# Kernel optimization log

Hardware: AMD Instinct MI355X
Metric: run time of the kernel (lower is better)

Reference implementation:

```python
import jax, jax.numpy as jnp
import numpy as np

B, N, DIM = 8, 1024, 768
HEADS, DHEAD = 12, 64
INNER = HEADS * DHEAD  # 768
ALPHA = 0.25
SCALE = DHEAD ** -0.5
EPS = 1e-5


def setup_inputs() -> dict:
    key = jax.random.key(0)
    ks = jax.random.split(key, 7)
    x = jax.random.normal(ks[0], (B, N, DIM), dtype=jnp.float32)
    h = jax.random.normal(ks[1], (B, HEADS, N, N), dtype=jnp.float32)
    gamma = jnp.ones((DIM,), dtype=jnp.float32)
    beta = jnp.zeros((DIM,), dtype=jnp.float32)
    w_qkv = jax.random.normal(ks[2], (DIM, 3 * INNER), dtype=jnp.float32) * (DIM ** -0.5)
    w_out = jax.random.normal(ks[3], (INNER, DIM), dtype=jnp.float32) * (INNER ** -0.5)
    b_out = jnp.zeros((DIM,), dtype=jnp.float32)
    return {"x": x, "h": h, "gamma": gamma, "beta": beta,
            "w_qkv": w_qkv, "w_out": w_out, "b_out": b_out}


def reference(x, h, gamma, beta, w_qkv, w_out, b_out):
    # LayerNorm over last dim
    mu = jnp.mean(x, axis=-1, keepdims=True)
    var = jnp.mean(jnp.square(x - mu), axis=-1, keepdims=True)
    xn = (x - mu) * jax.lax.rsqrt(var + EPS) * gamma + beta
    # fused QKV projection (no bias)
    qkv = xn @ w_qkv                                     # (b, n, 3*inner)
    q, k, v = jnp.split(qkv, 3, axis=-1)
    split_heads = lambda t: t.reshape(B, N, HEADS, DHEAD).transpose(0, 2, 1, 3)  # b h n d
    q, k, v = split_heads(q), split_heads(k), split_heads(v)
    raw = jnp.einsum('bhid,bhjd->bhij', q, k) * SCALE    # (b, h, n, n)
    blended = ALPHA * raw + (1.0 - ALPHA) * h
    attn = jax.nn.softmax(blended, axis=-1)              # dropout p=0 -> identity
    out = jnp.einsum('bhij,bhjd->bhid', attn, v)         # (b, h, n, d)
    out = out.transpose(0, 2, 1, 3).reshape(B, N, INNER)
    out = out @ w_out + b_out
    return (out, blended)
```

## Files before the change

kernel.cpp:

```cpp
#include <hip/hip_runtime.h>
#include <hip/hip_bf16.h>
#include <stdint.h>

#define NB 8
#define NSEQ 1024
#define DIMM 768
#define NHEADS 12
#define DH 64
#define NQKV 2304
#define ALPHA_ 0.25f
#define SCALE_ 0.125f
#define EPS_ 1e-5f

typedef __bf16 bf16;
typedef bf16 bf16x8 __attribute__((ext_vector_type(8)));
typedef bf16 bf16x4 __attribute__((ext_vector_type(4)));
typedef float f32x4 __attribute__((ext_vector_type(4)));

#define MFMA16(a, b, c) __builtin_amdgcn_mfma_f32_16x16x32_bf16((a), (b), (c), 0, 0, 0)

static __device__ __forceinline__ void load_lds16(const void* gsrc, void* ldst) {
  __builtin_amdgcn_global_load_lds(
      (__attribute__((address_space(1))) void*)gsrc,
      (__attribute__((address_space(3))) void*)ldst, 16, 0, 0);
}

#define BAR_LGKM()                                             \
  do {                                                         \
    __builtin_amdgcn_sched_barrier(0);                         \
    asm volatile("s_waitcnt lgkmcnt(0)" ::: "memory");         \
    __builtin_amdgcn_s_barrier();                              \
    __builtin_amdgcn_sched_barrier(0);                         \
  } while (0)

static __device__ __forceinline__ int swz(int row, int cb) {
  return cb ^ ((((row & 7) ^ ((cb >> 7) & 7)) << 4));
}

__global__ __launch_bounds__(256) void ln_kernel(
    const float* __restrict__ x, const float* __restrict__ gamma,
    const float* __restrict__ beta, bf16* __restrict__ xn) {
  const int row = blockIdx.x * 4 + (threadIdx.x >> 6);
  const int lane = threadIdx.x & 63;
  const float* xr = x + (size_t)row * DIMM;
  float4 v[3];
  float s = 0.f, s2 = 0.f;
#pragma unroll
  for (int c = 0; c < 3; ++c) {
    v[c] = *reinterpret_cast<const float4*>(xr + c * 256 + lane * 4);
    s += v[c].x + v[c].y + v[c].z + v[c].w;
    s2 += v[c].x * v[c].x + v[c].y * v[c].y + v[c].z * v[c].z + v[c].w * v[c].w;
  }
#pragma unroll
  for (int m = 1; m < 64; m <<= 1) {
    s += __shfl_xor(s, m);
    s2 += __shfl_xor(s2, m);
  }
  const float mu = s * (1.f / DIMM);
  const float rstd = rsqrtf(s2 * (1.f / DIMM) - mu * mu + EPS_);
#pragma unroll
  for (int c = 0; c < 3; ++c) {
    const float4 g4 = *reinterpret_cast<const float4*>(gamma + c * 256 + lane * 4);
    const float4 b4 = *reinterpret_cast<const float4*>(beta + c * 256 + lane * 4);
    bf16x4 o;
    o[0] = (bf16)((v[c].x - mu) * rstd * g4.x + b4.x);
    o[1] = (bf16)((v[c].y - mu) * rstd * g4.y + b4.y);
    o[2] = (bf16)((v[c].z - mu) * rstd * g4.z + b4.z);
    o[3] = (bf16)((v[c].w - mu) * rstd * g4.w + b4.w);
    *reinterpret_cast<bf16x4*>(xn + (size_t)row * DIMM + c * 256 + lane * 4) = o;
  }
}

__global__ __launch_bounds__(256) void tcast_kernel(
    const float* __restrict__ in, bf16* __restrict__ out, int R, int C) {
  __shared__ float tile[32][33];
  const int tx = threadIdx.x & 31, ty = threadIdx.x >> 5;
  const int c0 = blockIdx.x * 32, r0 = blockIdx.y * 32;
#pragma unroll
  for (int i = ty; i < 32; i += 8)
    tile[i][tx] = in[(size_t)(r0 + i) * C + c0 + tx];
  __syncthreads();
#pragma unroll
  for (int i = ty; i < 32; i += 8)
    out[(size_t)(c0 + i) * R + r0 + tx] = (bf16)tile[tx][i];
}

__global__ __launch_bounds__(256) void qkv_gemm(
    const bf16* __restrict__ xn, const bf16* __restrict__ wT,
    bf16* __restrict__ qb, bf16* __restrict__ kb, bf16* __restrict__ vt) {
  __shared__ __align__(16) bf16 As[128 * 32];
  __shared__ __align__(16) bf16 Bs[128 * 32];
  const int tid = threadIdx.x;
  const int wv = tid >> 6, l = tid & 63;
  const int l16 = l & 15, q4 = l >> 4;
  const int wr = wv >> 1, wc = wv & 1;
  const int c0 = blockIdx.x * 128, row0 = blockIdx.y * 128;
  const int sr = tid >> 2, skk = (tid & 3) * 8;
  f32x4 acc[4][4];
#pragma unroll
  for (int m = 0; m < 4; ++m)
#pragma unroll
    for (int n = 0; n < 4; ++n) acc[m][n] = f32x4{0.f, 0.f, 0.f, 0.f};
  for (int k0 = 0; k0 < DIMM; k0 += 32) {
    __syncthreads();
    load_lds16(xn + (size_t)(row0 + sr) * DIMM + k0 + skk, As + tid * 8);
    load_lds16(xn + (size_t)(row0 + 64 + sr) * DIMM + k0 + skk, As + 2048 + tid * 8);
    load_lds16(wT + (size_t)(c0 + sr) * DIMM + k0 + skk, Bs + tid * 8);
    load_lds16(wT + (size_t)(c0 + 64 + sr) * DIMM + k0 + skk, Bs + 2048 + tid * 8);
    __syncthreads();
    bf16x8 a[4], b[4];
#pragma unroll
    for (int m = 0; m < 4; ++m)
      a[m] = *reinterpret_cast<const bf16x8*>(&As[(wr * 64 + m * 16 + l16) * 32 + q4 * 8]);
#pragma unroll
    for (int n = 0; n < 4; ++n)
      b[n] = *reinterpret_cast<const bf16x8*>(&Bs[(wc * 64 + n * 16 + l16) * 32 + q4 * 8]);
#pragma unroll
    for (int m = 0; m < 4; ++m)
#pragma unroll
      for (int n = 0; n < 4; ++n) acc[m][n] = MFMA16(a[m], b[n], acc[m][n]);
  }
  const int sect = c0 / DIMM;
#pragma unroll
  for (int n = 0; n < 4; ++n) {
    const int gc = c0 + wc * 64 + n * 16 + l16;
    const int head = (gc % DIMM) >> 6;
    const int dd = gc & 63;
#pragma unroll
    for (int m = 0; m < 4; ++m) {
#pragma unroll
      for (int r = 0; r < 4; ++r) {
        const int gm = row0 + wr * 64 + m * 16 + q4 * 4 + r;
        const int b_ = gm >> 10, nn = gm & 1023;
        const size_t bhh = (size_t)b_ * NHEADS + head;
        const bf16 val = (bf16)acc[m][n][r];
        if (sect == 0)      qb[(bhh * NSEQ + nn) * DH + dd] = val;
        else if (sect == 1) kb[(bhh * NSEQ + nn) * DH + dd] = val;
        else                vt[(bhh * DH + dd) * NSEQ + nn] = val;
      }
    }
  }
}

__global__ __launch_bounds__(256, 4) void attn_kernel(
    const bf16* __restrict__ qb, const bf16* __restrict__ kb,
    const bf16* __restrict__ vt, const float* __restrict__ h,
    float* __restrict__ blended, bf16* __restrict__ attn_out) {
  __shared__ __align__(16) char S_lds[16 * 2176];
  __shared__ float lred[16];

  const int tid = threadIdx.x;
  const int wv = tid >> 6, l = tid & 63;
  const int l16 = l & 15, q4 = l >> 4;
  const int i0 = blockIdx.x * 16;
  const int bh = blockIdx.y;
  const int jb = wv * 256;

  const float* hbase = h + ((size_t)bh << 20);
  float* bbase = blended + ((size_t)bh << 20);

  bf16x8 qT[2];
#pragma unroll
  for (int w2 = 0; w2 < 2; ++w2)
    qT[w2] = *reinterpret_cast<const bf16x8*>(
        qb + ((size_t)bh * NSEQ + i0 + l16) * DH + w2 * 32 + q4 * 8);

  float4 hv0[4], hv1[4];
#pragma unroll
  for (int t = 0; t < 4; ++t) {
    hv0[t] = *reinterpret_cast<const float4*>(
        hbase + (size_t)(i0 + wv * 4 + 0) * NSEQ + t * 256 + l * 4);
    hv1[t] = *reinterpret_cast<const float4*>(
        hbase + (size_t)(i0 + wv * 4 + 1) * NSEQ + t * 256 + l * 4);
  }

  const bf16* kq = kb + ((size_t)bh * NSEQ + jb + l16) * DH + q4 * 8;
  char* srow_w = S_lds + l16 * 2176;
#pragma unroll
  for (int st = 0; st < 4; ++st) {
    f32x4 s[4];
#pragma unroll
    for (int js = 0; js < 4; ++js) s[js] = f32x4{0.f, 0.f, 0.f, 0.f};
#pragma unroll
    for (int js = 0; js < 4; ++js) {
#pragma unroll
      for (int w2 = 0; w2 < 2; ++w2) {
        const bf16x8 kf = *reinterpret_cast<const bf16x8*>(
            kq + (size_t)(st * 64 + js * 16) * DH + w2 * 32);
        s[js] = MFMA16(kf, qT[w2], s[js]);
      }
    }
#pragma unroll
    for (int js = 0; js < 4; ++js) {
      bf16x4 pk;
#pragma unroll
      for (int r = 0; r < 4; ++r) pk[r] = (bf16)(s[js][r] * (ALPHA_ * SCALE_));
      const int cb = (jb + st * 64 + js * 16 + q4 * 4) * 2;
      *reinterpret_cast<bf16x4*>(srow_w + swz(l16, cb)) = pk;
    }
  }

  float4 hv2[4], hv3[4];
#pragma unroll
  for (int t = 0; t < 4; ++t) {
    hv2[t] = *reinterpret_cast<const float4*>(
        hbase + (size_t)(i0 + wv * 4 + 2) * NSEQ + t * 256 + l * 4);
    hv3[t] = *reinterpret_cast<const float4*>(
        hbase + (size_t)(i0 + wv * 4 + 3) * NSEQ + t * 256 + l * 4);
  }

  BAR_LGKM();

  auto ROW = [&](int rr, float4* hv) {
    const int row = wv * 4 + rr;
    char* srow = S_lds + row * 2176;
    bf16x4 sv[4];
#pragma unroll
    for (int t = 0; t < 4; ++t)
      sv[t] = *reinterpret_cast<const bf16x4*>(srow + swz(row, t * 512 + l * 8));
    float4 bl[4];
    float tm = -1e30f;
#pragma unroll
    for (int t = 0; t < 4; ++t) {
      bl[t].x = fmaf(0.75f, hv[t].x, (float)sv[t][0]);
      bl[t].y = fmaf(0.75f, hv[t].y, (float)sv[t][1]);
      bl[t].z = fmaf(0.75f, hv[t].z, (float)sv[t][2]);
      bl[t].w = fmaf(0.75f, hv[t].w, (float)sv[t][3]);
      *reinterpret_cast<float4*>(
          bbase + (size_t)(i0 + row) * NSEQ + t * 256 + l * 4) = bl[t];
      tm = fmaxf(tm, fmaxf(fmaxf(bl[t].x, bl[t].y), fmaxf(bl[t].z, bl[t].w)));
    }
#pragma unroll
    for (int mm = 1; mm < 64; mm <<= 1) tm = fmaxf(tm, __shfl_xor(tm, mm));
    float rs = 0.f;
#pragma unroll
    for (int t = 0; t < 4; ++t) {
      bf16x4 pk;
      const float p0 = __expf(bl[t].x - tm); rs += p0; pk[0] = (bf16)p0;
      const float p1 = __expf(bl[t].y - tm); rs += p1; pk[1] = (bf16)p1;
      const float p2 = __expf(bl[t].z - tm); rs += p2; pk[2] = (bf16)p2;
      const float p3 = __expf(bl[t].w - tm); rs += p3; pk[3] = (bf16)p3;
      *reinterpret_cast<bf16x4*>(srow + swz(row, t * 512 + l * 8)) = pk;
    }
#pragma unroll
    for (int mm = 1; mm < 64; mm <<= 1) rs += __shfl_xor(rs, mm);
    if (l == 0) lred[row] = rs;
  };
  ROW(0, hv0);
  ROW(1, hv1);
  ROW(2, hv2);
  ROW(3, hv3);

  BAR_LGKM();

  const bf16* vq = vt + ((size_t)bh * DH + wv * 16 + l16) * NSEQ + q4 * 8;
  char* prow = S_lds + l16 * 2176;
  f32x4 a0 = f32x4{0.f, 0.f, 0.f, 0.f}, a1 = a0, a2 = a0, a3 = a0;
#pragma unroll
  for (int ks = 0; ks < 32; ks += 4) {
    const bf16x8 pa0 = *reinterpret_cast<const bf16x8*>(prow + swz(l16, (ks + 0) * 64 + q4 * 16));
    const bf16x8 vf0 = *reinterpret_cast<const bf16x8*>(vq + (ks + 0) * 32);
    a0 = MFMA16(pa0, vf0, a0);
    const bf16x8 pa1 = *reinterpret_cast<const bf16x8*>(prow + swz(l16, (ks + 1) * 64 + q4 * 16));
    const bf16x8 vf1 = *reinterpret_cast<const bf16x8*>(vq + (ks + 1) * 32);
    a1 = MFMA16(pa1, vf1, a1);
    const bf16x8 pa2 = *reinterpret_cast<const bf16x8*>(prow + swz(l16, (ks + 2) * 64 + q4 * 16));
    const bf16x8 vf2 = *reinterpret_cast<const bf16x8*>(vq + (ks + 2) * 32);
    a2 = MFMA16(pa2, vf2, a2);
    const bf16x8 pa3 = *reinterpret_cast<const bf16x8*>(prow + swz(l16, (ks + 3) * 64 + q4 * 16));
    const bf16x8 vf3 = *reinterpret_cast<const bf16x8*>(vq + (ks + 3) * 32);
    a3 = MFMA16(pa3, vf3, a3);
  }
  const f32x4 af = (a0 + a1) + (a2 + a3);
  const int b = bh / NHEADS, head = bh % NHEADS;
#pragma unroll
  for (int r = 0; r < 4; ++r) {
    const int q = q4 * 4 + r;
    attn_out[((size_t)b * NSEQ + i0 + q) * DIMM + head * DH + wv * 16 + l16] =
        (bf16)(af[r] / lred[q]);
  }
}

__global__ __launch_bounds__(256) void oproj_gemm(
    const bf16* __restrict__ ain, const bf16* __restrict__ wT,
    const float* __restrict__ bias, float* __restrict__ out) {
  __shared__ __align__(16) bf16 As[128 * 32];
  __shared__ __align__(16) bf16 Bs[128 * 32];
  const int tid = threadIdx.x;
  const int wv = tid >> 6, l = tid & 63;
  const int l16 = l & 15, q4 = l >> 4;
  const int wr = wv >> 1, wc = wv & 1;
  const int c0 = blockIdx.x * 128, row0 = blockIdx.y * 128;
  const int sr = tid >> 2, skk = (tid & 3) * 8;
  f32x4 acc[4][4];
#pragma unroll
  for (int m = 0; m < 4; ++m)
#pragma unroll
    for (int n = 0; n < 4; ++n) acc[m][n] = f32x4{0.f, 0.f, 0.f, 0.f};
  for (int k0 = 0; k0 < DIMM; k0 += 32) {
    __syncthreads();
    load_lds16(ain + (size_t)(row0 + sr) * DIMM + k0 + skk, As + tid * 8);
    load_lds16(ain + (size_t)(row0 + 64 + sr) * DIMM + k0 + skk, As + 2048 + tid * 8);
    load_lds16(wT + (size_t)(c0 + sr) * DIMM + k0 + skk, Bs + tid * 8);
    load_lds16(wT + (size_t)(c0 + 64 + sr) * DIMM + k0 + skk, Bs + 2048 + tid * 8);
    __syncthreads();
    bf16x8 a[4], b[4];
#pragma unroll
    for (int m = 0; m < 4; ++m)
      a[m] = *reinterpret_cast<const bf16x8*>(&As[(wr * 64 + m * 16 + l16) * 32 + q4 * 8]);
#pragma unroll
    for (int n = 0; n < 4; ++n)
      b[n] = *reinterpret_cast<const bf16x8*>(&Bs[(wc * 64 + n * 16 + l16) * 32 + q4 * 8]);
#pragma unroll
    for (int m = 0; m < 4; ++m)
#pragma unroll
      for (int n = 0; n < 4; ++n) acc[m][n] = MFMA16(a[m], b[n], acc[m][n]);
  }
#pragma unroll
  for (int n = 0; n < 4; ++n) {
    const int gc = c0 + wc * 64 + n * 16 + l16;
    const float bv = bias[gc];
#pragma unroll
    for (int m = 0; m < 4; ++m) {
#pragma unroll
      for (int r = 0; r < 4; ++r) {
        const int gm = row0 + wr * 64 + m * 16 + q4 * 4 + r;
        out[(size_t)gm * DIMM + gc] = acc[m][n][r] + bv;
      }
    }
  }
}

extern "C" void kernel_launch(void* const* d_in, const int* in_sizes, int n_in,
                              void* d_out, int out_size, void* d_ws, size_t ws_size,
                              hipStream_t stream) {
  const float* x = (const float*)d_in[0];
  const float* h = (const float*)d_in[1];
  const float* gamma = (const float*)d_in[2];
  const float* beta = (const float*)d_in[3];
  const float* w_qkv = (const float*)d_in[4];
  const float* w_out = (const float*)d_in[5];
  const float* b_out = (const float*)d_in[6];
  float* out = (float*)d_out;
  float* blended = out + (size_t)NB * NSEQ * DIMM;

  char* ws = (char*)d_ws;
  bf16* xn = (bf16*)(ws);
  bf16* qb = (bf16*)(ws + 12582912);
  bf16* kb = (bf16*)(ws + 25165824);
  bf16* vt = (bf16*)(ws + 37748736);
  bf16* wqkvT = (bf16*)(ws + 50331648);
  bf16* woutT = (bf16*)(ws + 53870592);

  hipLaunchKernelGGL(ln_kernel, dim3(2048), dim3(256), 0, stream, x, gamma, beta, xn);
  hipLaunchKernelGGL(tcast_kernel, dim3(72, 24), dim3(256), 0, stream, w_qkv, wqkvT, DIMM, NQKV);
  hipLaunchKernelGGL(tcast_kernel, dim3(24, 24), dim3(256), 0, stream, w_out, woutT, DIMM, DIMM);
  hipLaunchKernelGGL(qkv_gemm, dim3(18, 64), dim3(256), 0, stream, xn, wqkvT, qb, kb, vt);
  hipLaunchKernelGGL(attn_kernel, dim3(64, 96), dim3(256), 0, stream, qb, kb, vt, h, blended, xn);
  hipLaunchKernelGGL(oproj_gemm, dim3(6, 64), dim3(256), 0, stream, xn, woutT, b_out, out);
}
```

Measured before the change: 388.0 us.

## Split fused attention into score GEMM, blend/softmax-sum, and PV GEMM kernels

```diff
diff --git a/kernel.cpp b/kernel.cpp
--- a/kernel.cpp
+++ b/kernel.cpp
@@ -23,18 +23,6 @@
   __builtin_amdgcn_global_load_lds(
       (__attribute__((address_space(1))) void*)gsrc,
       (__attribute__((address_space(3))) void*)ldst, 16, 0, 0);
-}
-
-#define BAR_LGKM()                                             \
-  do {                                                         \
-    __builtin_amdgcn_sched_barrier(0);                         \
-    asm volatile("s_waitcnt lgkmcnt(0)" ::: "memory");         \
-    __builtin_amdgcn_s_barrier();                              \
-    __builtin_amdgcn_sched_barrier(0);                         \
-  } while (0)
-
-static __device__ __forceinline__ int swz(int row, int cb) {
-  return cb ^ ((((row & 7) ^ ((cb >> 7) & 7)) << 4));
 }
 
 __global__ __launch_bounds__(256) void ln_kernel(
@@ -142,13 +130,9 @@
   }
 }
 
-__global__ __launch_bounds__(256, 4) void attn_kernel(
+__global__ __launch_bounds__(256) void s_gemm(
     const bf16* __restrict__ qb, const bf16* __restrict__ kb,
-    const bf16* __restrict__ vt, const float* __restrict__ h,
-    float* __restrict__ blended, bf16* __restrict__ attn_out) {
-  __shared__ __align__(16) char S_lds[16 * 2176];
-  __shared__ float lred[16];
-
+    float* __restrict__ blended) {
   const int tid = threadIdx.x;
   const int wv = tid >> 6, l = tid & 63;
   const int l16 = l & 15, q4 = l >> 4;
@@ -156,26 +140,14 @@
   const int bh = blockIdx.y;
   const int jb = wv * 256;
 
-  const float* hbase = h + ((size_t)bh << 20);
-  float* bbase = blended + ((size_t)bh << 20);
-
   bf16x8 qT[2];
 #pragma unroll
   for (int w2 = 0; w2 < 2; ++w2)
     qT[w2] = *reinterpret_cast<const bf16x8*>(
         qb + ((size_t)bh * NSEQ + i0 + l16) * DH + w2 * 32 + q4 * 8);
 
-  float4 hv0[4], hv1[4];
-#pragma unroll
-  for (int t = 0; t < 4; ++t) {
-    hv0[t] = *reinterpret_cast<const float4*>(
-        hbase + (size_t)(i0 + wv * 4 + 0) * NSEQ + t * 256 + l * 4);
-    hv1[t] = *reinterpret_cast<const float4*>(
-        hbase + (size_t)(i0 + wv * 4 + 1) * NSEQ + t * 256 + l * 4);
-  }
-
   const bf16* kq = kb + ((size_t)bh * NSEQ + jb + l16) * DH + q4 * 8;
-  char* srow_w = S_lds + l16 * 2176;
+  char* sdst = (char*)blended + (size_t)((bh << 10) + i0 + l16) * 4096;
 #pragma unroll
   for (int st = 0; st < 4; ++st) {
     f32x4 s[4];
@@ -195,89 +167,107 @@
       bf16x4 pk;
 #pragma unroll
       for (int r = 0; r < 4; ++r) pk[r] = (bf16)(s[js][r] * (ALPHA_ * SCALE_));
-      const int cb = (jb + st * 64 + js * 16 + q4 * 4) * 2;
-      *reinterpret_cast<bf16x4*>(srow_w + swz(l16, cb)) = pk;
-    }
-  }
-
-  float4 hv2[4], hv3[4];
-#pragma unroll
-  for (int t = 0; t < 4; ++t) {
-    hv2[t] = *reinterpret_cast<const float4*>(
-        hbase + (size_t)(i0 + wv * 4 + 2) * NSEQ + t * 256 + l * 4);
-    hv3[t] = *reinterpret_cast<const float4*>(
-        hbase + (size_t)(i0 + wv * 4 + 3) * NSEQ + t * 256 + l * 4);
-  }
-
-  BAR_LGKM();
-
-  auto ROW = [&](int rr, float4* hv) {
-    const int row = wv * 4 + rr;
-    char* srow = S_lds + row * 2176;
-    bf16x4 sv[4];
-#pragma unroll
-    for (int t = 0; t < 4; ++t)
-      sv[t] = *reinterpret_cast<const bf16x4*>(srow + swz(row, t * 512 + l * 8));
-    float4 bl[4];
-    float tm = -1e30f;
+      *reinterpret_cast<bf16x4*>(sdst + (jb + st * 64 + js * 16 + q4 * 4) * 2) = pk;
+    }
+  }
+}
+
+__global__ __launch_bounds__(256) void blend_kernel(
+    const float* __restrict__ h, float* __restrict__ blended,
+    float* __restrict__ lsum) {
+  const int l = threadIdx.x & 63;
+  const int w = blockIdx.x * 4 + (threadIdx.x >> 6);
+  float4 hA[4], hB[4];
+  bf16x4 sA[4], sB[4];
+
+  auto LOAD = [&](int rid, float4* hv, bf16x4* sv) {
+    const float* hp = h + (size_t)rid * 1024;
+    const char* sp = (const char*)blended + (size_t)rid * 4096;
+#pragma unroll
+    for (int c = 0; c < 4; ++c) {
+      hv[c] = *reinterpret_cast<const float4*>(hp + c * 256 + l * 4);
+      sv[c] = *reinterpret_cast<const bf16x4*>(sp + (c * 256 + l * 4) * 2);
+    }
+  };
+  auto COMP = [&](int rid, const float4* hv, const bf16x4* sv) {
+    float* bp = blended + (size_t)rid * 1024;
+    float ls = 0.f;
+#pragma unroll
+    for (int c = 0; c < 4; ++c) {
+      float4 b;
+      b.x = fmaf(0.75f, hv[c].x, (float)sv[c][0]);
+      b.y = fmaf(0.75f, hv[c].y, (float)sv[c][1]);
+      b.z = fmaf(0.75f, hv[c].z, (float)sv[c][2]);
+      b.w = fmaf(0.75f, hv[c].w, (float)sv[c][3]);
+      *reinterpret_cast<float4*>(bp + c * 256 + l * 4) = b;
+      ls += __expf(b.x) + __expf(b.y) + __expf(b.z) + __expf(b.w);
+    }
+#pragma unroll
+    for (int mm = 1; mm < 64; mm <<= 1) ls += __shfl_xor(ls, mm);
+    if (l == 0) lsum[rid] = ls;
+  };
+
+  LOAD(w, hA, sA);
+#pragma unroll 1
+  for (int it = 0; it < 16; it += 2) {
+    LOAD(w + (it + 1) * 6144, hB, sB);
+    COMP(w + it * 6144, hA, sA);
+    if (it + 2 < 16) LOAD(w + (it + 2) * 6144, hA, sA);
+    COMP(w + (it + 1) * 6144, hB, sB);
+  }
+}
+
+__global__ __launch_bounds__(256) void pv_gemm(
+    const float* __restrict__ blended, const bf16* __restrict__ vt,
+    const float* __restrict__ lsum, bf16* __restrict__ attn_out) {
+  __shared__ __align__(16) float ored[4 * 16 * 64];
+  const int tid = threadIdx.x;
+  const int wv = tid >> 6, l = tid & 63;
+  const int l16 = l & 15, q4 = l >> 4;
+  const int i0 = blockIdx.x * 16;
+  const int bh = blockIdx.y;
+
+  const float* bq = blended + (size_t)((bh << 10) + i0 + l16) * 1024 + q4 * 8;
+  const bf16* vbase = vt + (size_t)bh * DH * NSEQ + (size_t)q4 * 8;
+
+  f32x4 acc[4];
+#pragma unroll
+  for (int f = 0; f < 4; ++f) acc[f] = f32x4{0.f, 0.f, 0.f, 0.f};
+
+#pragma unroll
+  for (int k8 = 0; k8 < 8; ++k8) {
+    const int ks = wv * 8 + k8;
+    const f32x4 u0 = *reinterpret_cast<const f32x4*>(bq + ks * 32);
+    const f32x4 u1 = *reinterpret_cast<const f32x4*>(bq + ks * 32 + 4);
+    bf16x8 pa;
 #pragma unroll
     for (int t = 0; t < 4; ++t) {
-      bl[t].x = fmaf(0.75f, hv[t].x, (float)sv[t][0]);
-      bl[t].y = fmaf(0.75f, hv[t].y, (float)sv[t][1]);
-      bl[t].z = fmaf(0.75f, hv[t].z, (float)sv[t][2]);
-      bl[t].w = fmaf(0.75f, hv[t].w, (float)sv[t][3]);
-      *reinterpret_cast<float4*>(
-          bbase + (size_t)(i0 + row) * NSEQ + t * 256 + l * 4) = bl[t];
-      tm = fmaxf(tm, fmaxf(fmaxf(bl[t].x, bl[t].y), fmaxf(bl[t].z, bl[t].w)));
-    }
-#pragma unroll
-    for (int mm = 1; mm < 64; mm <<= 1) tm = fmaxf(tm, __shfl_xor(tm, mm));
-    float rs = 0.f;
-#pragma unroll
-    for (int t = 0; t < 4; ++t) {
-      bf16x4 pk;
-      const float p0 = __expf(bl[t].x - tm); rs += p0; pk[0] = (bf16)p0;
-      const float p1 = __expf(bl[t].y - tm); rs += p1; pk[1] = (bf16)p1;
-      const float p2 = __expf(bl[t].z - tm); rs += p2; pk[2] = (bf16)p2;
-      const float p3 = __expf(bl[t].w - tm); rs += p3; pk[3] = (bf16)p3;
-      *reinterpret_cast<bf16x4*>(srow + swz(row, t * 512 + l * 8)) = pk;
-    }
-#pragma unroll
-    for (int mm = 1; mm < 64; mm <<= 1) rs += __shfl_xor(rs, mm);
-    if (l == 0) lred[row] = rs;
-  };
-  ROW(0, hv0);
-  ROW(1, hv1);
-  ROW(2, hv2);
-  ROW(3, hv3);
-
-  BAR_LGKM();
-
-  const bf16* vq = vt + ((size_t)bh * DH + wv * 16 + l16) * NSEQ + q4 * 8;
-  char* prow = S_lds + l16 * 2176;
-  f32x4 a0 = f32x4{0.f, 0.f, 0.f, 0.f}, a1 = a0, a2 = a0, a3 = a0;
-#pragma unroll
-  for (int ks = 0; ks < 32; ks += 4) {
-    const bf16x8 pa0 = *reinterpret_cast<const bf16x8*>(prow + swz(l16, (ks + 0) * 64 + q4 * 16));
-    const bf16x8 vf0 = *reinterpret_cast<const bf16x8*>(vq + (ks + 0) * 32);
-    a0 = MFMA16(pa0, vf0, a0);
-    const bf16x8 pa1 = *reinterpret_cast<const bf16x8*>(prow + swz(l16, (ks + 1) * 64 + q4 * 16));
-    const bf16x8 vf1 = *reinterpret_cast<const bf16x8*>(vq + (ks + 1) * 32);
-    a1 = MFMA16(pa1, vf1, a1);
-    const bf16x8 pa2 = *reinterpret_cast<const bf16x8*>(prow + swz(l16, (ks + 2) * 64 + q4 * 16));
-    const bf16x8 vf2 = *reinterpret_cast<const bf16x8*>(vq + (ks + 2) * 32);
-    a2 = MFMA16(pa2, vf2, a2);
-    const bf16x8 pa3 = *reinterpret_cast<const bf16x8*>(prow + swz(l16, (ks + 3) * 64 + q4 * 16));
-    const bf16x8 vf3 = *reinterpret_cast<const bf16x8*>(vq + (ks + 3) * 32);
-    a3 = MFMA16(pa3, vf3, a3);
-  }
-  const f32x4 af = (a0 + a1) + (a2 + a3);
+      pa[t] = (bf16)__expf(u0[t]);
+      pa[4 + t] = (bf16)__expf(u1[t]);
+    }
+#pragma unroll
+    for (int f = 0; f < 4; ++f) {
+      const bf16x8 vf = *reinterpret_cast<const bf16x8*>(
+          vbase + (size_t)(f * 16 + l16) * NSEQ + ks * 32);
+      acc[f] = MFMA16(pa, vf, acc[f]);
+    }
+  }
+
+#pragma unroll
+  for (int f = 0; f < 4; ++f)
+#pragma unroll
+    for (int r = 0; r < 4; ++r)
+      ored[(wv * 16 + q4 * 4 + r) * 64 + f * 16 + l16] = acc[f][r];
+  __syncthreads();
+
   const int b = bh / NHEADS, head = bh % NHEADS;
 #pragma unroll
-  for (int r = 0; r < 4; ++r) {
-    const int q = q4 * 4 + r;
-    attn_out[((size_t)b * NSEQ + i0 + q) * DIMM + head * DH + wv * 16 + l16] =
-        (bf16)(af[r] / lred[q]);
+  for (int c = 0; c < 4; ++c) {
+    const int row = wv * 4 + c;
+    float o = ored[(0 * 16 + row) * 64 + l] + ored[(1 * 16 + row) * 64 + l] +
+              ored[(2 * 16 + row) * 64 + l] + ored[(3 * 16 + row) * 64 + l];
+    o /= lsum[(bh << 10) + i0 + row];
+    attn_out[((size_t)b * NSEQ + i0 + row) * DIMM + head * DH + l] = (bf16)o;
   }
 }
 
@@ -351,11 +341,14 @@
   bf16* vt = (bf16*)(ws + 37748736);
   bf16* wqkvT = (bf16*)(ws + 50331648);
   bf16* woutT = (bf16*)(ws + 53870592);
+  float* lsum = (float*)(ws + 55050240);
 
   hipLaunchKernelGGL(ln_kernel, dim3(2048), dim3(256), 0, stream, x, gamma, beta, xn);
   hipLaunchKernelGGL(tcast_kernel, dim3(72, 24), dim3(256), 0, stream, w_qkv, wqkvT, DIMM, NQKV);
   hipLaunchKernelGGL(tcast_kernel, dim3(24, 24), dim3(256), 0, stream, w_out, woutT, DIMM, DIMM);
   hipLaunchKernelGGL(qkv_gemm, dim3(18, 64), dim3(256), 0, stream, xn, wqkvT, qb, kb, vt);
-  hipLaunchKernelGGL(attn_kernel, dim3(64, 96), dim3(256), 0, stream, qb, kb, vt, h, blended, xn);
+  hipLaunchKernelGGL(s_gemm, dim3(64, 96), dim3(256), 0, stream, qb, kb, blended);
+  hipLaunchKernelGGL(blend_kernel, dim3(1536), dim3(256), 0, stream, h, blended, lsum);
+  hipLaunchKernelGGL(pv_gemm, dim3(64, 96), dim3(256), 0, stream, blended, vt, lsum, xn);
   hipLaunchKernelGGL(oproj_gemm, dim3(6, 64), dim3(256), 0, stream, xn, woutT, b_out, out);
 }
```

New measurement: 601.1 us. 1.55x slower.
